# Optimization experiments

Hardware: AMD Instinct MI355X
Metric: run time of the kernel (lower is better)

Reference implementation:

```python
import jax, jax.numpy as jnp
import numpy as np

N_NODES = 100000


def _sage_conv(x, src, dst, w_l, b_l, w_r):
    # PyG SAGEConv (aggr='mean', root_weight=True):
    #   out = lin_l(mean_{j in N(i)} x_j) + lin_r(x_i)
    # messages flow src (row 0) -> dst (row 1)
    msgs = x[src]                                             # [E, d]
    agg = jax.ops.segment_sum(msgs, dst, num_segments=N_NODES)  # [N, d]
    cnt = jax.ops.segment_sum(jnp.ones((src.shape[0], 1), x.dtype), dst,
                              num_segments=N_NODES)           # [N, 1]
    mean = agg / jnp.maximum(cnt, 1.0)
    return mean @ w_l + b_l + x @ w_r


def setup_inputs() -> dict:
    key = jax.random.key(0)
    ks = jax.random.split(key, 8)
    in_dim, hid, out = 128, 64, 128
    n_edges = 1600000
    x = jax.random.normal(ks[0], (N_NODES, in_dim), dtype=jnp.float32)
    edge_index = jax.random.randint(ks[1], (2, n_edges), 0, N_NODES, dtype=jnp.int64)
    s1 = 1.0 / np.sqrt(in_dim)
    s2 = 1.0 / np.sqrt(hid)
    return {
        "x": x,
        "edge_index": edge_index,
        "w1_l": jax.random.uniform(ks[2], (in_dim, hid), jnp.float32, -s1, s1),
        "b1": jnp.zeros((hid,), jnp.float32),
        "w1_r": jax.random.uniform(ks[3], (in_dim, hid), jnp.float32, -s1, s1),
        "w2_l": jax.random.uniform(ks[4], (hid, out), jnp.float32, -s2, s2),
        "b2": jnp.zeros((out,), jnp.float32),
        "w2_r": jax.random.uniform(ks[5], (hid, out), jnp.float32, -s2, s2),
    }


def reference(x, edge_index, w1_l, b1, w1_r, w2_l, b2, w2_r):
    src, dst = edge_index[0], edge_index[1]
    h = jax.nn.relu(_sage_conv(x, src, dst, w1_l, b1, w1_r))
    h = _sage_conv(h, src, dst, w2_l, b2, w2_r)
    return h
```

## Files before the change

kernel.cpp:

```cpp
#include <hip/hip_runtime.h>

#define N_NODES 100000
#define NBUCK   782
#define P1TILE  4096
#define SLAB    4096
#define AGG_CAP 512

typedef __bf16 bf16x8 __attribute__((ext_vector_type(8)));
typedef float floatx4 __attribute__((ext_vector_type(4)));
typedef float floatx2 __attribute__((ext_vector_type(2)));

static __device__ __forceinline__ unsigned short f2bf(float f) {
  unsigned u = __float_as_uint(f);
  u += 0x7fff + ((u >> 16) & 1);
  return (unsigned short)(u >> 16);
}

__global__ __launch_bounds__(256) void init_kernel(
    int* __restrict__ bucket_cursor,
    const float* __restrict__ w1_l, const float* __restrict__ w1_r,
    const float* __restrict__ w2_l, const float* __restrict__ w2_r,
    unsigned short* __restrict__ Wt1, unsigned short* __restrict__ Wt2) {
  int gid = blockIdx.x * 256 + threadIdx.x;
  if (gid < NBUCK + 2) bucket_cursor[gid] = 0;
  int n = gid >> 7, k = gid & 127;
  float v1 = (n < 64) ? w1_l[k * 64 + n] : w1_r[k * 64 + (n - 64)];
  Wt1[n * 128 + k] = f2bf(v1);
  float v2 = (k < 64) ? w2_l[k * 128 + n] : w2_r[(k - 64) * 128 + n];
  Wt2[n * 128 + k] = f2bf(v2);
}

__global__ __launch_bounds__(512) void part_gemm1_kernel(
    const int* __restrict__ src, const int* __restrict__ dst,
    int* __restrict__ bucket_cursor, unsigned* __restrict__ pairs,
    int n_edges, int nb_part,
    const float* __restrict__ x, const unsigned short* __restrict__ Wt1,
    const float* __restrict__ b1, unsigned short* __restrict__ ZB1, int M) {
  __shared__ __align__(16) char smem[44224];
  int t = threadIdx.x;

  if ((int)blockIdx.x >= nb_part) {
    unsigned short* As = (unsigned short*)smem;
    int node0 = ((int)blockIdx.x - nb_part) * 128;
    #pragma unroll
    for (int i = 0; i < 8; ++i) {
      int c = t + i * 512;
      int row = c >> 5, c4 = (c & 31) * 4;
      float4 v = make_float4(0.f, 0.f, 0.f, 0.f);
      if (node0 + row < M) v = *(const float4*)&x[(long)(node0 + row) * 128 + c4];
      ushort4 o;
      o.x = f2bf(v.x); o.y = f2bf(v.y); o.z = f2bf(v.z); o.w = f2bf(v.w);
      *(ushort4*)&As[row * 136 + c4] = o;
    }
    __syncthreads();
    int w8 = t >> 6, lane = t & 63;
    int m = lane & 15, q = lane >> 4;
    int w = w8 & 3, half = w8 >> 2;
    int col0 = w * 32, rowbase = half * 64;
    floatx4 acc[4][2];
    #pragma unroll
    for (int rt = 0; rt < 4; ++rt)
      #pragma unroll
      for (int ct = 0; ct < 2; ++ct) acc[rt][ct] = (floatx4){0.f, 0.f, 0.f, 0.f};
    #pragma unroll
    for (int ks = 0; ks < 4; ++ks) {
      bf16x8 b0 = *(const bf16x8*)&Wt1[(col0 + m) * 128 + ks * 32 + q * 8];
      bf16x8 bb = *(const bf16x8*)&Wt1[(col0 + 16 + m) * 128 + ks * 32 + q * 8];
      #pragma unroll
      for (int rt = 0; rt < 4; ++rt) {
        bf16x8 a = *(const bf16x8*)&As[(rowbase + rt * 16 + m) * 136 + ks * 32 + q * 8];
        acc[rt][0] = __builtin_amdgcn_mfma_f32_16x16x32_bf16(a, b0, acc[rt][0], 0, 0, 0);
        acc[rt][1] = __builtin_amdgcn_mfma_f32_16x16x32_bf16(a, bb, acc[rt][1], 0, 0, 0);
      }
    }
    #pragma unroll
    for (int ct = 0; ct < 2; ++ct) {
      int col = col0 + ct * 16 + m;
      float bv = (col >= 64) ? b1[col - 64] : 0.f;
      #pragma unroll
      for (int rt = 0; rt < 4; ++rt) {
        #pragma unroll
        for (int i = 0; i < 4; ++i) {
          int row = node0 + rowbase + rt * 16 + q * 4 + i;
          if (row >= M) continue;
          ZB1[(long)row * 128 + col] = f2bf(acc[rt][ct][i] + bv);
        }
      }
    }
    return;
  }

  int2* sorted = (int2*)smem;
  int* hist  = (int*)(smem + 32768);
  int* scan_ = hist + NBUCK;
  int* gbase = scan_ + NBUCK;
  int* tmp   = gbase + NBUCK;
  long e0 = (long)blockIdx.x * P1TILE;
  int n = (int)min((long)P1TILE, (long)n_edges - e0);

  for (int b = t; b < NBUCK; b += 512) hist[b] = 0;
  __syncthreads();
  for (int i = t; i < n; i += 512) atomicAdd(&hist[dst[e0 + i] >> 7], 1);
  __syncthreads();

  int loc[2];
  int s = 0;
  #pragma unroll
  for (int j = 0; j < 2; ++j) {
    int idx = 2 * t + j;
    loc[j] = s;
    s += (idx < NBUCK) ? hist[idx] : 0;
  }
  tmp[t] = s;
  __syncthreads();
  for (int off = 1; off < 512; off <<= 1) {
    int u = (t >= off) ? tmp[t - off] : 0;
    __syncthreads();
    tmp[t] += u;
    __syncthreads();
  }
  int excl = tmp[t] - s;
  #pragma unroll
  for (int j = 0; j < 2; ++j) {
    int idx = 2 * t + j;
    if (idx < NBUCK) scan_[idx] = excl + loc[j];
  }
  __syncthreads();

  for (int b = t; b < NBUCK; b += 512) {
    int c = hist[b];
    gbase[b] = c ? atomicAdd(&bucket_cursor[b], c) : 0;
    hist[b] = scan_[b];
  }
  __syncthreads();

  for (int i = t; i < n; i += 512) {
    int sv = src[e0 + i];
    int dv = dst[e0 + i];
    int r = atomicAdd(&hist[dv >> 7], 1);
    sorted[r] = make_int2(sv, dv);
  }
  __syncthreads();

  for (int i = t; i < n; i += 512) {
    int2 p = sorted[i];
    int b = p.y >> 7;
    int pos = gbase[b] + (i - scan_[b]);
    if (pos < SLAB) {
      unsigned pk = (unsigned)p.x | ((unsigned)(p.y & 127) << 17);
      pairs[(long)b * SLAB + pos] = pk;
    }
  }
}

__global__ __launch_bounds__(512) void bucket_csr_kernel(
    const unsigned* __restrict__ pairs, const int* __restrict__ bucket_cnt,
    int2* __restrict__ offsets2, int* __restrict__ src_sorted, int n_nodes) {
  __shared__ unsigned sp[SLAB];
  __shared__ int lout[SLAB];
  __shared__ int ndeg[128];
  __shared__ int nsc[128];
  int b = blockIdx.x;
  int node0 = b << 7;
  int t = threadIdx.x;
  long sbeg = (long)b * SLAB;
  int m = min(bucket_cnt[b], SLAB);
  if (t < 128) ndeg[t] = 0;
  __syncthreads();

  for (int i = t; i < m; i += 512) {
    unsigned p = pairs[sbeg + i];
    sp[i] = p;
    atomicAdd(&ndeg[p >> 17], 1);
  }
  __syncthreads();

  if (t < 128) nsc[t] = ndeg[t];
  __syncthreads();
  for (int off = 1; off < 128; off <<= 1) {
    int u = 0;
    if (t < 128 && t >= off) u = nsc[t - off];
    __syncthreads();
    if (t < 128) nsc[t] += u;
    __syncthreads();
  }
  if (t < 128) {
    int excl = nsc[t] - ndeg[t];
    int node = node0 + t;
    if (node < n_nodes)
      offsets2[node] = make_int2((int)sbeg + excl, (int)sbeg + nsc[t]);
    ndeg[t] = excl;
  }
  __syncthreads();

  for (int i = t; i < m; i += 512) {
    unsigned p = sp[i];
    int r = atomicAdd(&ndeg[p >> 17], 1);
    lout[r] = (int)(p & 0x1FFFFu);
  }
  __syncthreads();
  for (int i = t; i < m; i += 512) src_sorted[sbeg + i] = lout[i];
}

__global__ __launch_bounds__(256) void mfma_gemm2_kernel(
    const unsigned short* __restrict__ A, const unsigned short* __restrict__ Wt,
    const float* __restrict__ bias, float* __restrict__ Y, int M) {
  __shared__ unsigned short As[64 * 136];
  int node0 = blockIdx.x * 64;
  int t = threadIdx.x;
  #pragma unroll
  for (int i = 0; i < 4; ++i) {
    int c = t + i * 256;
    int row = c >> 4, c8 = (c & 15) * 8;
    uint4 v = make_uint4(0u, 0u, 0u, 0u);
    if (node0 + row < M) v = *(const uint4*)&A[(long)(node0 + row) * 128 + c8];
    *(uint4*)&As[row * 136 + c8] = v;
  }
  __syncthreads();
  int w = t >> 6, lane = t & 63;
  int m = lane & 15, q = lane >> 4;
  int col0 = w * 32;
  floatx4 acc[4][2];
  #pragma unroll
  for (int rt = 0; rt < 4; ++rt)
    #pragma unroll
    for (int ct = 0; ct < 2; ++ct) acc[rt][ct] = (floatx4){0.f, 0.f, 0.f, 0.f};

  #pragma unroll
  for (int ks = 0; ks < 4; ++ks) {
    bf16x8 b0 = *(const bf16x8*)&Wt[(col0 + m) * 128 + ks * 32 + q * 8];
    bf16x8 b1 = *(const bf16x8*)&Wt[(col0 + 16 + m) * 128 + ks * 32 + q * 8];
    #pragma unroll
    for (int rt = 0; rt < 4; ++rt) {
      bf16x8 a = *(const bf16x8*)&As[(rt * 16 + m) * 136 + ks * 32 + q * 8];
      acc[rt][0] = __builtin_amdgcn_mfma_f32_16x16x32_bf16(a, b0, acc[rt][0], 0, 0, 0);
      acc[rt][1] = __builtin_amdgcn_mfma_f32_16x16x32_bf16(a, b1, acc[rt][1], 0, 0, 0);
    }
  }
  #pragma unroll
  for (int ct = 0; ct < 2; ++ct) {
    int col = col0 + ct * 16 + m;
    float bv = bias[col];
    #pragma unroll
    for (int rt = 0; rt < 4; ++rt) {
      #pragma unroll
      for (int i = 0; i < 4; ++i) {
        int row = node0 + rt * 16 + q * 4 + i;
        if (row >= M) continue;
        Y[(long)row * 128 + col] = acc[rt][ct][i] + bv;
      }
    }
  }
}

#define ACC_P(A, v)                                                            \
  do {                                                                         \
    A[0] += (floatx2){__uint_as_float((v).x << 16),                            \
                      __uint_as_float((v).x & 0xffff0000u)};                   \
    A[1] += (floatx2){__uint_as_float((v).y << 16),                            \
                      __uint_as_float((v).y & 0xffff0000u)};                   \
    A[2] += (floatx2){__uint_as_float((v).z << 16),                            \
                      __uint_as_float((v).z & 0xffff0000u)};                   \
    A[3] += (floatx2){__uint_as_float((v).w << 16),                            \
                      __uint_as_float((v).w & 0xffff0000u)};                   \
  } while (0)

template <bool FUSE_RELU>
__global__ __launch_bounds__(256) void aggregate_bf16_kernel(
    const unsigned short* __restrict__ gsrc, const unsigned short* __restrict__ zadd,
    unsigned short* __restrict__ outp, const int2* __restrict__ offsets2,
    const int* __restrict__ src_sorted, int n_nodes) {
  __shared__ int stage[4 * AGG_CAP];
  int wv = threadIdx.x >> 6;
  int lane = threadIdx.x & 63;
  int wid = (blockIdx.x << 2) | wv;
  int node8 = wid << 3;
  int sub = lane >> 3;
  int sl  = lane & 7;
  int node = node8 + sub;
  bool wvalid = (node8 < n_nodes);
  bool nvalid = wvalid && (node < n_nodes);

  int wbeg = 0, wend = 0, beg = 0, end = 0;
  if (wvalid) {
    wbeg = offsets2[node8].x;
    wend = offsets2[min(node8 + 8, n_nodes) - 1].y;
  }
  if (nvalid) {
    int2 o = offsets2[node];
    beg = o.x; end = o.y;
  }
  int deg = end - beg;
  int cnt = wend - wbeg;
  int* my = &stage[wv * AGG_CAP];
  bool staged = wvalid && (cnt <= AGG_CAP);
  if (staged) {
    for (int i = lane; i < cnt; i += 64) my[i] = src_sorted[wbeg + i];
  }
  __syncthreads();

  const unsigned short* base = gsrc + sl * 8;
  floatx2 A0[4], A1[4], A2[4], A3[4];
  #pragma unroll
  for (int i = 0; i < 4; ++i) {
    A0[i] = (floatx2){0.f, 0.f}; A1[i] = (floatx2){0.f, 0.f};
    A2[i] = (floatx2){0.f, 0.f}; A3[i] = (floatx2){0.f, 0.f};
  }

  if (staged) {
    int lb = beg - wbeg;
    int e = 0;
    for (; e + 8 <= deg; e += 8) {
      int s0 = my[lb + e];
      int s1 = my[lb + e + 1];
      int s2 = my[lb + e + 2];
      int s3 = my[lb + e + 3];
      int s4 = my[lb + e + 4];
      int s5 = my[lb + e + 5];
      int s6 = my[lb + e + 6];
      int s7 = my[lb + e + 7];
      uint4 v0 = *(const uint4*)(base + (long)s0 * 128);
      uint4 v1 = *(const uint4*)(base + (long)s1 * 128);
      uint4 v2 = *(const uint4*)(base + (long)s2 * 128);
      uint4 v3 = *(const uint4*)(base + (long)s3 * 128);
      uint4 v4 = *(const uint4*)(base + (long)s4 * 128);
      uint4 v5 = *(const uint4*)(base + (long)s5 * 128);
      uint4 v6 = *(const uint4*)(base + (long)s6 * 128);
      uint4 v7 = *(const uint4*)(base + (long)s7 * 128);
      ACC_P(A0, v0); ACC_P(A1, v1); ACC_P(A2, v2); ACC_P(A3, v3);
      ACC_P(A0, v4); ACC_P(A1, v5); ACC_P(A2, v6); ACC_P(A3, v7);
    }
    if (e + 4 <= deg) {
      int s0 = my[lb + e];
      int s1 = my[lb + e + 1];
      int s2 = my[lb + e + 2];
      int s3 = my[lb + e + 3];
      uint4 v0 = *(const uint4*)(base + (long)s0 * 128);
      uint4 v1 = *(const uint4*)(base + (long)s1 * 128);
      uint4 v2 = *(const uint4*)(base + (long)s2 * 128);
      uint4 v3 = *(const uint4*)(base + (long)s3 * 128);
      ACC_P(A0, v0); ACC_P(A1, v1); ACC_P(A2, v2); ACC_P(A3, v3);
      e += 4;
    }
    for (; e < deg; ++e) {
      int s0 = my[lb + e];
      uint4 v0 = *(const uint4*)(base + (long)s0 * 128);
      ACC_P(A0, v0);
    }
  } else if (nvalid) {
    for (int e = beg; e < end; ++e) {
      int s0 = src_sorted[e];
      uint4 v0 = *(const uint4*)(base + (long)s0 * 128);
      ACC_P(A0, v0);
    }
  }
  #pragma unroll
  for (int i = 0; i < 4; ++i) A0[i] = (A0[i] + A1[i]) + (A2[i] + A3[i]);

  if (nvalid) {
    float inv = 1.f / fmaxf((float)deg, 1.f);
    float r[8];
    r[0] = A0[0].x * inv; r[1] = A0[0].y * inv;
    r[2] = A0[1].x * inv; r[3] = A0[1].y * inv;
    r[4] = A0[2].x * inv; r[5] = A0[2].y * inv;
    r[6] = A0[3].x * inv; r[7] = A0[3].y * inv;
    if (FUSE_RELU) {
      uint4 z = *(const uint4*)&zadd[(long)node * 128 + sl * 8];
      r[0] = fmaxf(r[0] + __uint_as_float(z.x << 16), 0.f);
      r[1] = fmaxf(r[1] + __uint_as_float(z.x & 0xffff0000u), 0.f);
      r[2] = fmaxf(r[2] + __uint_as_float(z.y << 16), 0.f);
      r[3] = fmaxf(r[3] + __uint_as_float(z.y & 0xffff0000u), 0.f);
      r[4] = fmaxf(r[4] + __uint_as_float(z.z << 16), 0.f);
      r[5] = fmaxf(r[5] + __uint_as_float(z.z & 0xffff0000u), 0.f);
      r[6] = fmaxf(r[6] + __uint_as_float(z.w << 16), 0.f);
      r[7] = fmaxf(r[7] + __uint_as_float(z.w & 0xffff0000u), 0.f);
    }
    uint4 ov;
    ov.x = (unsigned)f2bf(r[0]) | ((unsigned)f2bf(r[1]) << 16);
    ov.y = (unsigned)f2bf(r[2]) | ((unsigned)f2bf(r[3]) << 16);
    ov.z = (unsigned)f2bf(r[4]) | ((unsigned)f2bf(r[5]) << 16);
    ov.w = (unsigned)f2bf(r[6]) | ((unsigned)f2bf(r[7]) << 16);
    *(uint4*)&outp[(long)node * 128 + sl * 8] = ov;
  }
}
#undef ACC_P

extern "C" void kernel_launch(void* const* d_in, const int* in_sizes, int n_in,
                              void* d_out, int out_size, void* d_ws, size_t ws_size,
                              hipStream_t stream) {
  const float* x    = (const float*)d_in[0];
  const int*   ei   = (const int*)d_in[1];
  const float* w1_l = (const float*)d_in[2];
  const float* b1   = (const float*)d_in[3];
  const float* w1_r = (const float*)d_in[4];
  const float* w2_l = (const float*)d_in[5];
  const float* b2   = (const float*)d_in[6];
  const float* w2_r = (const float*)d_in[7];
  float* out = (float*)d_out;

  const int E = in_sizes[1] / 2;
  const int* src = ei;
  const int* dst = ei + E;

  unsigned short* ZB1 = (unsigned short*)d_ws;
  unsigned short* ZB2 = ZB1 + (long)N_NODES * 128;
  unsigned short* Wt1 = ZB2 + (long)N_NODES * 128;
  unsigned short* Wt2 = Wt1 + 16384;
  int* bucket_cursor = (int*)(Wt2 + 16384);
  int2* offsets2     = (int2*)(bucket_cursor + NBUCK + 2);
  int* src_sorted    = (int*)(offsets2 + N_NODES);
  unsigned* pairs    = (unsigned*)(src_sorted + (long)NBUCK * SLAB);

  int nb_part = (E + P1TILE - 1) / P1TILE;
  int gemm1_blocks = (N_NODES + 127) / 128;

  init_kernel<<<64, 256, 0, stream>>>(bucket_cursor, w1_l, w1_r, w2_l, w2_r,
                                      Wt1, Wt2);
  part_gemm1_kernel<<<nb_part + gemm1_blocks, 512, 0, stream>>>(
      src, dst, bucket_cursor, pairs, E, nb_part, x, Wt1, b1, ZB1, N_NODES);
  bucket_csr_kernel<<<NBUCK, 512, 0, stream>>>(pairs, bucket_cursor,
                                               offsets2, src_sorted, N_NODES);

  int agg_blocks = (N_NODES + 31) / 32;
  aggregate_bf16_kernel<true><<<agg_blocks, 256, 0, stream>>>(
      ZB1, ZB1 + 64, ZB2 + 64, offsets2, src_sorted, N_NODES);
  aggregate_bf16_kernel<false><<<agg_blocks, 256, 0, stream>>>(
      ZB2 + 64, nullptr, ZB2, offsets2, src_sorted, N_NODES);
  mfma_gemm2_kernel<<<(N_NODES + 63) / 64, 256, 0, stream>>>(
      ZB2, Wt2, b2, out, N_NODES);
}
```

Before: 237.7 us.

## Replace global bucket atomics with per-tile local sorts and offset tables

The partition phase no longer reserves slots in global per-bucket cursors with atomics and scatters pairs into bucket slabs. Each edge tile now writes its locally bucket-sorted packed pairs contiguously, along with its per-bucket scan table. The CSR kernel then gathers each bucket's edges from all tiles using a prefix sum over tile counts and a binary search per element. This removes global atomics and the scattered writes, and shrinks shared memory in the partition kernel. In exchange the CSR kernel does more strided reads (tiles × buckets table) and per-element binary searches.

```diff
diff --git a/kernel.cpp b/kernel.cpp
--- a/kernel.cpp
+++ b/kernel.cpp
@@ -3,6 +3,8 @@
 #define N_NODES 100000
 #define NBUCK   782
 #define P1TILE  4096
+#define NTILES  391
+#define SCNW    783
 #define SLAB    4096
 #define AGG_CAP 512
 
@@ -17,12 +19,10 @@
 }
 
 __global__ __launch_bounds__(256) void init_kernel(
-    int* __restrict__ bucket_cursor,
     const float* __restrict__ w1_l, const float* __restrict__ w1_r,
     const float* __restrict__ w2_l, const float* __restrict__ w2_r,
     unsigned short* __restrict__ Wt1, unsigned short* __restrict__ Wt2) {
   int gid = blockIdx.x * 256 + threadIdx.x;
-  if (gid < NBUCK + 2) bucket_cursor[gid] = 0;
   int n = gid >> 7, k = gid & 127;
   float v1 = (n < 64) ? w1_l[k * 64 + n] : w1_r[k * 64 + (n - 64)];
   Wt1[n * 128 + k] = f2bf(v1);
@@ -32,11 +32,11 @@
 
 __global__ __launch_bounds__(512) void part_gemm1_kernel(
     const int* __restrict__ src, const int* __restrict__ dst,
-    int* __restrict__ bucket_cursor, unsigned* __restrict__ pairs,
+    unsigned* __restrict__ pairs, int* __restrict__ scn,
     int n_edges, int nb_part,
     const float* __restrict__ x, const unsigned short* __restrict__ Wt1,
     const float* __restrict__ b1, unsigned short* __restrict__ ZB1, int M) {
-  __shared__ __align__(16) char smem[44224];
+  __shared__ __align__(16) char smem[34816];
   int t = threadIdx.x;
 
   if ((int)blockIdx.x >= nb_part) {
@@ -90,12 +90,12 @@
     return;
   }
 
-  int2* sorted = (int2*)smem;
-  int* hist  = (int*)(smem + 32768);
+  unsigned* sorted_u = (unsigned*)smem;
+  int* hist  = (int*)(smem + 16384);
   int* scan_ = hist + NBUCK;
-  int* gbase = scan_ + NBUCK;
-  int* tmp   = gbase + NBUCK;
-  long e0 = (long)blockIdx.x * P1TILE;
+  int* tmp   = scan_ + NBUCK;
+  int tile = (int)blockIdx.x;
+  long e0 = (long)tile * P1TILE;
   int n = (int)min((long)P1TILE, (long)n_edges - e0);
 
   for (int b = t; b < NBUCK; b += 512) hist[b] = 0;
@@ -127,49 +127,66 @@
   }
   __syncthreads();
 
-  for (int b = t; b < NBUCK; b += 512) {
-    int c = hist[b];
-    gbase[b] = c ? atomicAdd(&bucket_cursor[b], c) : 0;
-    hist[b] = scan_[b];
-  }
-  __syncthreads();
-
+  for (int b = t; b < SCNW; b += 512)
+    scn[(long)tile * SCNW + b] = (b < NBUCK) ? scan_[b] : n;
+
+  for (int b = t; b < NBUCK; b += 512) hist[b] = scan_[b];
+  __syncthreads();
   for (int i = t; i < n; i += 512) {
     int sv = src[e0 + i];
     int dv = dst[e0 + i];
     int r = atomicAdd(&hist[dv >> 7], 1);
-    sorted[r] = make_int2(sv, dv);
-  }
-  __syncthreads();
-
-  for (int i = t; i < n; i += 512) {
-    int2 p = sorted[i];
-    int b = p.y >> 7;
-    int pos = gbase[b] + (i - scan_[b]);
-    if (pos < SLAB) {
-      unsigned pk = (unsigned)p.x | ((unsigned)(p.y & 127) << 17);
-      pairs[(long)b * SLAB + pos] = pk;
-    }
-  }
+    sorted_u[r] = (unsigned)sv | ((unsigned)(dv & 127) << 17);
+  }
+  __syncthreads();
+  for (int i = t; i < n; i += 512)
+    pairs[(long)tile * P1TILE + i] = sorted_u[i];
 }
 
 __global__ __launch_bounds__(512) void bucket_csr_kernel(
-    const unsigned* __restrict__ pairs, const int* __restrict__ bucket_cnt,
-    int2* __restrict__ offsets2, int* __restrict__ src_sorted, int n_nodes) {
+    const unsigned* __restrict__ pairs, const int* __restrict__ scn,
+    int2* __restrict__ offsets2, int* __restrict__ src_sorted,
+    int n_nodes, int ntiles) {
   __shared__ unsigned sp[SLAB];
   __shared__ int lout[SLAB];
   __shared__ int ndeg[128];
   __shared__ int nsc[128];
+  __shared__ int tlo[NTILES];
+  __shared__ int tpref[513];
+  __shared__ int tmp[512];
   int b = blockIdx.x;
   int node0 = b << 7;
   int t = threadIdx.x;
   long sbeg = (long)b * SLAB;
-  int m = min(bucket_cnt[b], SLAB);
+
+  int cnt_t = 0;
+  if (t < ntiles) {
+    int lo = scn[(long)t * SCNW + b];
+    int hi = scn[(long)t * SCNW + b + 1];
+    tlo[t] = lo;
+    cnt_t = hi - lo;
+  }
+  tmp[t] = cnt_t;
   if (t < 128) ndeg[t] = 0;
   __syncthreads();
+  for (int off = 1; off < 512; off <<= 1) {
+    int u = (t >= off) ? tmp[t - off] : 0;
+    __syncthreads();
+    tmp[t] += u;
+    __syncthreads();
+  }
+  if (t == 0) tpref[0] = 0;
+  tpref[t + 1] = tmp[t];
+  __syncthreads();
+  int m = min(tpref[ntiles], SLAB);
 
   for (int i = t; i < m; i += 512) {
-    unsigned p = pairs[sbeg + i];
+    int lo = 0, hi = ntiles - 1;
+    while (lo < hi) {
+      int mid = (lo + hi + 1) >> 1;
+      if (tpref[mid] <= i) lo = mid; else hi = mid - 1;
+    }
+    unsigned p = pairs[(long)lo * P1TILE + tlo[lo] + (i - tpref[lo])];
     sp[i] = p;
     atomicAdd(&ndeg[p >> 17], 1);
   }
@@ -402,24 +419,24 @@
   const int* src = ei;
   const int* dst = ei + E;
 
+  int ntiles = (E + P1TILE - 1) / P1TILE;
+
   unsigned short* ZB1 = (unsigned short*)d_ws;
   unsigned short* ZB2 = ZB1 + (long)N_NODES * 128;
   unsigned short* Wt1 = ZB2 + (long)N_NODES * 128;
   unsigned short* Wt2 = Wt1 + 16384;
-  int* bucket_cursor = (int*)(Wt2 + 16384);
-  int2* offsets2     = (int2*)(bucket_cursor + NBUCK + 2);
+  int2* offsets2     = (int2*)(Wt2 + 16384);
   int* src_sorted    = (int*)(offsets2 + N_NODES);
   unsigned* pairs    = (unsigned*)(src_sorted + (long)NBUCK * SLAB);
-
-  int nb_part = (E + P1TILE - 1) / P1TILE;
+  int* scn           = (int*)(pairs + (long)ntiles * P1TILE);
+
   int gemm1_blocks = (N_NODES + 127) / 128;
 
-  init_kernel<<<64, 256, 0, stream>>>(bucket_cursor, w1_l, w1_r, w2_l, w2_r,
-                                      Wt1, Wt2);
-  part_gemm1_kernel<<<nb_part + gemm1_blocks, 512, 0, stream>>>(
-      src, dst, bucket_cursor, pairs, E, nb_part, x, Wt1, b1, ZB1, N_NODES);
-  bucket_csr_kernel<<<NBUCK, 512, 0, stream>>>(pairs, bucket_cursor,
-                                               offsets2, src_sorted, N_NODES);
+  init_kernel<<<64, 256, 0, stream>>>(w1_l, w1_r, w2_l, w2_r, Wt1, Wt2);
+  part_gemm1_kernel<<<ntiles + gemm1_blocks, 512, 0, stream>>>(
+      src, dst, pairs, scn, E, ntiles, x, Wt1, b1, ZB1, N_NODES);
+  bucket_csr_kernel<<<NBUCK, 512, 0, stream>>>(pairs, scn, offsets2,
+                                               src_sorted, N_NODES, ntiles);
 
   int agg_blocks = (N_NODES + 31) / 32;
   aggregate_bf16_kernel<true><<<agg_blocks, 256, 0, stream>>>(
```

Result: no change. 242.3 us (+2.0%).
